# Optimization experiments

Hardware: AMD Instinct MI355X
Metric: run time of the kernel (lower is better)

## Reference

```python
import jax, jax.numpy as jnp
import numpy as np

N, K, D = 8192, 64, 256          # nodes, edges per dst node, feat_dim
RATE = 0.5                        # denoise_topK_rate
SET0 = int(K * (1.0 - RATE))      # edges dropped per row (lowest keep-prob)


def setup_inputs() -> dict:
    key = jax.random.key(0)
    ks = jax.random.split(key, 6)
    # K unique, sorted neighbors per row (sorted => pair ordering matches
    # torch's row-major nonzero() on a dense adjacency)
    nbr = jax.vmap(lambda k: jax.random.permutation(k, N)[:K])(
        jax.random.split(ks[0], N))
    nbr = jnp.sort(nbr, axis=1).astype(jnp.int32)
    vals = jax.random.uniform(ks[1], (N, K), minval=0.1, maxval=1.0)
    adj = jnp.zeros((N, N), jnp.float32).at[jnp.arange(N)[:, None], nbr].set(vals)
    feat = jax.random.normal(ks[2], (N, D), dtype=jnp.float32)
    # keep_cls params: Linear(D, D//2) -> PReLU(D//2) -> Linear(D//2, 2)
    W1 = jax.random.normal(ks[3], (D, D // 2), dtype=jnp.float32) / np.float32(np.sqrt(D))
    b1 = jnp.zeros((D // 2,), jnp.float32)
    prelu_a = jnp.full((D // 2,), 0.25, jnp.float32)  # torch PReLU default init
    W2 = jax.random.normal(ks[4], (D // 2, 2), dtype=jnp.float32) / np.float32(np.sqrt(D // 2))
    b2 = jnp.zeros((2,), jnp.float32)
    return {"adj": adj, "feat": feat, "nbr_idx": nbr, "dst_num": N,
            "W1": W1, "b1": b1, "prelu_a": prelu_a, "W2": W2, "b2": b2}


def reference(adj, feat, nbr_idx, dst_num, W1, b1, prelu_a, W2, b2):
    dst = dst_num  # == adj.shape[0]; every dst row has exactly K nonzeros
    rows = jnp.arange(dst, dtype=jnp.int32)[:, None]            # [dst,1]
    pair_src = jnp.repeat(jnp.arange(dst, dtype=jnp.int32), K)  # [E]
    pair_dst = nbr_idx.reshape(-1)                              # [E]
    pair_list = jnp.stack([pair_src, pair_dst], axis=1)         # [E,2]
    before_edge_num = jnp.float32(pair_list.shape[0]) / dst

    # edge MLP on feature differences
    diff = feat[pair_src] - feat[pair_dst]                      # [E,D]
    h = diff @ W1 + b1
    h = jnp.where(h >= 0, h, prelu_a * h)                       # PReLU
    prob_arr = jax.nn.softmax(h @ W2 + b2, axis=1)              # [E,2]

    # segmented (per-dst-row) argsort of keep-prob; drop SET0 lowest
    p1 = prob_arr[:, 1].reshape(dst, K)                         # [dst,K]
    order = jnp.argsort(p1, axis=1)                             # ascending
    drop_cols = jnp.take_along_axis(nbr_idx, order[:, :SET0], axis=1)
    adj2 = adj.at[rows, drop_cols].set(0.0)
    left_row = (rows * K + order[:, SET0:]).reshape(-1)         # kept edge ids
    after_edge_num = jnp.count_nonzero(adj2).astype(jnp.float32) / dst

    # degree-normalize
    degrees = jnp.sum(adj2, axis=1)
    new_adj = adj2 / (degrees[:, None] + 1e-6)
    return (new_adj, feat, prob_arr, pair_list, before_edge_num,
            after_edge_num, left_row)
```

## Files before the change

kernel.cpp:

```cpp
#include <hip/hip_runtime.h>
#include <cmath>

#define NN 8192
#define KK 64
#define DD 256
#define HH 128
#define SET0V 32
#define EE (NN*KK)

typedef float f4_t __attribute__((ext_vector_type(4)));

static constexpr size_t OFF_ADJ  = 0;
static constexpr size_t OFF_FEAT = (size_t)NN * NN;
static constexpr size_t OFF_PROB = OFF_FEAT + (size_t)NN * DD;
static constexpr size_t OFF_PAIR = OFF_PROB + (size_t)EE * 2;
static constexpr size_t OFF_BEF  = OFF_PAIR + (size_t)EE * 2;
static constexpr size_t OFF_AFT  = OFF_BEF + 1;
static constexpr size_t OFF_LEFT = OFF_AFT + 1;

__global__ __launch_bounds__(128) void k_g(const float* __restrict__ feat,
                                           const float* __restrict__ W1,
                                           double* __restrict__ g,
                                           f4_t* __restrict__ out_feat,
                                           float* __restrict__ out_scal) {
  __shared__ float sf[8 * DD];
  int j = threadIdx.x;
  int n0 = blockIdx.x * 8;
  const f4_t* fsrc = (const f4_t*)(feat + (size_t)n0 * DD);
  f4_t* fdst = (f4_t*)sf;
  f4_t* odst = out_feat + (size_t)n0 * DD / 4;
#pragma unroll
  for (int t = 0; t < 4; t++) {
    f4_t v = fsrc[j + t * 128];
    fdst[j + t * 128] = v;
    __builtin_nontemporal_store(v, odst + j + t * 128);
  }
  if (blockIdx.x == 0 && j == 0) {
    out_scal[0] = 64.0f;
    out_scal[1] = 32.0f;
  }
  __syncthreads();
  double acc[8];
#pragma unroll
  for (int n = 0; n < 8; n++) acc[n] = 0.0;
  for (int k = 0; k < DD; k += 4) {
    double w0 = (double)W1[(k + 0) * HH + j];
    double w1 = (double)W1[(k + 1) * HH + j];
    double w2 = (double)W1[(k + 2) * HH + j];
    double w3 = (double)W1[(k + 3) * HH + j];
#pragma unroll
    for (int n = 0; n < 8; n++) {
      f4_t f = *(const f4_t*)&sf[n * DD + k];
      acc[n] += (double)f.x * w0;
      acc[n] += (double)f.y * w1;
      acc[n] += (double)f.z * w2;
      acc[n] += (double)f.w * w3;
    }
  }
#pragma unroll
  for (int n = 0; n < 8; n++) g[(size_t)(n0 + n) * HH + j] = acc[n];
}

__global__ __launch_bounds__(256) void k_main(
    const double* __restrict__ g, const int* __restrict__ nbr,
    const float* __restrict__ b1, const float* __restrict__ b2,
    const float* __restrict__ pa, const float* __restrict__ W2,
    const float* __restrict__ adj, float* __restrict__ out_adj,
    float* __restrict__ out_prob, float* __restrict__ out_pair,
    float* __restrict__ out_left) {
  int wave = threadIdx.x >> 6;
  int lane = threadIdx.x & 63;
  int r = blockIdx.x * 4 + wave;
  int q = lane >> 4;
  int s = lane & 15;

  const int* nrow = nbr + r * KK;
  int c_mine = nrow[lane];
  float v = __builtin_nontemporal_load(&adj[(size_t)r * NN + c_mine]);

  f4_t* row4 = (f4_t*)(out_adj + (size_t)r * NN);
  const f4_t z = {0.f, 0.f, 0.f, 0.f};

  double grb[8], aa[8], w0c[8], w1c[8];
  const double* gr = g + (size_t)r * HH + s * 8;
#pragma unroll
  for (int d = 0; d < 8; d++) {
    int dim = s * 8 + d;
    grb[d] = gr[d] + (double)b1[dim];
    aa[d]  = (double)pa[dim];
    w0c[d] = (double)W2[2 * dim];
    w1c[d] = (double)W2[2 * dim + 1];
  }

  double st0 = 0.0, st1 = 0.0;
  for (int grp = 0; grp < 16; grp++) {
    __builtin_nontemporal_store(z, row4 + lane + (2 * grp) * 64);
    __builtin_nontemporal_store(z, row4 + lane + (2 * grp + 1) * 64);

    int c = nrow[grp * 4 + q];
    const double* gc = g + (size_t)c * HH + s * 8;
    double t0 = 0.0, t1 = 0.0;
#pragma unroll
    for (int d = 0; d < 8; d++) {
      double h = grb[d] - gc[d];
      h = h >= 0.0 ? h : aa[d] * h;
      t0 += h * w0c[d];
      t1 += h * w1c[d];
    }
#pragma unroll
    for (int m = 1; m < 16; m <<= 1) {
      t0 += __shfl_xor(t0, m, 16);
      t1 += __shfl_xor(t1, m, 16);
    }
    if (s == grp) { st0 = t0; st1 = t1; }
  }
  int src = ((lane & 3) << 4) | (lane >> 2);
  double T0 = __shfl(st0, src, 64);
  double T1 = __shfl(st1, src, 64);
  double l0 = T0 + (double)b2[0];
  double l1 = T1 + (double)b2[1];
  double dkey = l1 - l0;

  size_t e = (size_t)r * KK + lane;
  float dm = (float)(l0 > l1 ? l0 : l1);
  float e0 = expf((float)l0 - dm), e1 = expf((float)l1 - dm);
  float inv = 1.0f / (e0 + e1);
  *(float2*)(out_prob + 2 * e) = make_float2(e0 * inv, e1 * inv);
  *(float2*)(out_pair + 2 * e) = make_float2((float)r, (float)c_mine);

  __shared__ double sp[4][64];
  __shared__ double sv[4][64];
  sp[wave][lane] = dkey;
  __syncthreads();
  int rank = 0;
#pragma unroll 8
  for (int j = 0; j < KK; j++) {
    double qq = sp[wave][j];
    rank += (int)((qq < dkey) || (qq == dkey && j < lane));
  }
  bool kept = rank >= SET0V;
  sv[wave][lane] = kept ? (double)v : 0.0;
  __syncthreads();
  double deg = 0.0;
#pragma unroll 8
  for (int j = 0; j < KK; j++) deg += sv[wave][j];
  if (kept) {
    out_adj[(size_t)r * NN + c_mine] = (float)((double)v / (deg + 1e-6));
    out_left[(size_t)r * SET0V + (rank - SET0V)] = (float)(r * KK + lane);
  }
}

extern "C" void kernel_launch(void* const* d_in, const int* in_sizes, int n_in,
                              void* d_out, int out_size, void* d_ws, size_t ws_size,
                              hipStream_t stream) {
  const float* adj  = (const float*)d_in[0];
  const float* feat = (const float*)d_in[1];
  const int*   nbr  = (const int*)d_in[2];
  const float* W1   = (const float*)d_in[4];
  const float* b1   = (const float*)d_in[5];
  const float* pa   = (const float*)d_in[6];
  const float* W2   = (const float*)d_in[7];
  const float* b2   = (const float*)d_in[8];
  float* out = (float*)d_out;

  double* g = (double*)d_ws;

  hipLaunchKernelGGL(k_g, dim3(1024), dim3(128), 0, stream,
                     feat, W1, g, (f4_t*)(out + OFF_FEAT), out + OFF_BEF);
  hipLaunchKernelGGL(k_main, dim3(2048), dim3(256), 0, stream,
                     g, nbr, b1, b2, pa, W2, adj,
                     out + OFF_ADJ, out + OFF_PROB, out + OFF_PAIR,
                     out + OFF_LEFT);
}
```

Measured before the change: 492.2 us.

## Split each adjacency row across two wavefronts to double parallelism

Each row is now handled by two waves, each computing the MLP logits for 32 of the 64 edges and zeroing half of the output row, with results exchanged through shared memory. The grid doubles to 4096 blocks, giving more waves in flight to hide gather latency on the g table and the streaming zero stores. In exchange, half the lanes sit idle in the softmax and output stages, and the rank loop is duplicated across both waves.

```diff
diff --git a/kernel.cpp b/kernel.cpp
--- a/kernel.cpp
+++ b/kernel.cpp
@@ -70,16 +70,16 @@
     float* __restrict__ out_left) {
   int wave = threadIdx.x >> 6;
   int lane = threadIdx.x & 63;
-  int r = blockIdx.x * 4 + wave;
+  int half = wave & 1;
+  int rloc = wave >> 1;
+  int r = blockIdx.x * 2 + rloc;
   int q = lane >> 4;
   int s = lane & 15;
 
   const int* nrow = nbr + r * KK;
-  int c_mine = nrow[lane];
+  int e_mine = 32 * half + (lane & 31);
+  int c_mine = nrow[e_mine];
   float v = __builtin_nontemporal_load(&adj[(size_t)r * NN + c_mine]);
-
-  f4_t* row4 = (f4_t*)(out_adj + (size_t)r * NN);
-  const f4_t z = {0.f, 0.f, 0.f, 0.f};
 
   double grb[8], aa[8], w0c[8], w1c[8];
   const double* gr = g + (size_t)r * HH + s * 8;
@@ -93,11 +93,8 @@
   }
 
   double st0 = 0.0, st1 = 0.0;
-  for (int grp = 0; grp < 16; grp++) {
-    __builtin_nontemporal_store(z, row4 + lane + (2 * grp) * 64);
-    __builtin_nontemporal_store(z, row4 + lane + (2 * grp + 1) * 64);
-
-    int c = nrow[grp * 4 + q];
+  for (int grp = 0; grp < 8; grp++) {
+    int c = nrow[32 * half + grp * 4 + q];
     const double* gc = g + (size_t)c * HH + s * 8;
     double t0 = 0.0, t1 = 0.0;
 #pragma unroll
@@ -114,39 +111,56 @@
     }
     if (s == grp) { st0 = t0; st1 = t1; }
   }
-  int src = ((lane & 3) << 4) | (lane >> 2);
-  double T0 = __shfl(st0, src, 64);
-  double T1 = __shfl(st1, src, 64);
-  double l0 = T0 + (double)b2[0];
-  double l1 = T1 + (double)b2[1];
-  double dkey = l1 - l0;
+  double l0 = st0 + (double)b2[0];
+  double l1 = st1 + (double)b2[1];
+  double dk = l1 - l0;
 
-  size_t e = (size_t)r * KK + lane;
-  float dm = (float)(l0 > l1 ? l0 : l1);
-  float e0 = expf((float)l0 - dm), e1 = expf((float)l1 - dm);
-  float inv = 1.0f / (e0 + e1);
-  *(float2*)(out_prob + 2 * e) = make_float2(e0 * inv, e1 * inv);
-  *(float2*)(out_pair + 2 * e) = make_float2((float)r, (float)c_mine);
+  __shared__ double sl0[2][64], sl1[2][64], sdk[2][64], sv[2][64];
+  if (s < 8) {
+    int el = 32 * half + 4 * s + q;
+    sl0[rloc][el] = l0;
+    sl1[rloc][el] = l1;
+    sdk[rloc][el] = dk;
+  }
 
-  __shared__ double sp[4][64];
-  __shared__ double sv[4][64];
-  sp[wave][lane] = dkey;
+  f4_t* row4 = (f4_t*)(out_adj + (size_t)r * NN) + half * 1024 + lane;
+  const f4_t z = {0.f, 0.f, 0.f, 0.f};
+#pragma unroll
+  for (int t = 0; t < 16; t++)
+    __builtin_nontemporal_store(z, row4 + t * 64);
+
   __syncthreads();
+
+  double L0 = sl0[rloc][e_mine];
+  double L1 = sl1[rloc][e_mine];
+  double dkey = sdk[rloc][e_mine];
+
+  if (lane < 32) {
+    size_t e = (size_t)r * KK + e_mine;
+    float dm = (float)(L0 > L1 ? L0 : L1);
+    float e0 = expf((float)L0 - dm), e1 = expf((float)L1 - dm);
+    float inv = 1.0f / (e0 + e1);
+    *(float2*)(out_prob + 2 * e) = make_float2(e0 * inv, e1 * inv);
+    *(float2*)(out_pair + 2 * e) = make_float2((float)r, (float)c_mine);
+  }
+
   int rank = 0;
 #pragma unroll 8
   for (int j = 0; j < KK; j++) {
-    double qq = sp[wave][j];
-    rank += (int)((qq < dkey) || (qq == dkey && j < lane));
+    double qq = sdk[rloc][j];
+    rank += (int)((qq < dkey) || (qq == dkey && j < e_mine));
   }
   bool kept = rank >= SET0V;
-  sv[wave][lane] = kept ? (double)v : 0.0;
+
+  if (lane < 32) sv[rloc][e_mine] = kept ? (double)v : 0.0;
   __syncthreads();
   double deg = 0.0;
 #pragma unroll 8
-  for (int j = 0; j < KK; j++) deg += sv[wave][j];
-  if (kept) {
+  for (int j = 0; j < KK; j++) deg += sv[rloc][j];
+
+  if (lane < 32 && kept) {
     out_adj[(size_t)r * NN + c_mine] = (float)((double)v / (deg + 1e-6));
-    out_left[(size_t)r * SET0V + (rank - SET0V)] = (float)(r * KK + lane);
+    out_left[(size_t)r * SET0V + (rank - SET0V)] = (float)(r * KK + e_mine);
   }
 }
 
@@ -167,7 +181,7 @@
 
   hipLaunchKernelGGL(k_g, dim3(1024), dim3(128), 0, stream,
                      feat, W1, g, (f4_t*)(out + OFF_FEAT), out + OFF_BEF);
-  hipLaunchKernelGGL(k_main, dim3(2048), dim3(256), 0, stream,
+  hipLaunchKernelGGL(k_main, dim3(4096), dim3(256), 0, stream,
                      g, nbr, b1, b2, pa, W2, adj,
                      out + OFF_ADJ, out + OFF_PROB, out + OFF_PAIR,
                      out + OFF_LEFT);
```

Result: slower. 512.8 us (+4.2%).
